# Kernel tuning notes

Hardware: AMD Instinct MI355X
Metric: run time of the kernel (lower is better)

## Reference

```python
import jax, jax.numpy as jnp
import numpy as np

B, S, H = 1, 2048, 2048
NH, NKV, HD = 16, 4, 128
N_REP = NH // NKV
WINDOW = 1024
THETA = 10000.0


def _rope(x, fc):
    # x: [B,S,h,HD]; fc: [B,S,HD//2,2] (cos,sin)
    xr = x.reshape(*x.shape[:-1], HD // 2, 2)
    a, b = xr[..., 0], xr[..., 1]
    cos = fc[:, :, None, :, 0]
    sin = fc[:, :, None, :, 1]
    out = jnp.stack((a * cos - b * sin, a * sin + b * cos), axis=-1)
    return out.reshape(x.shape)


def setup_inputs() -> dict:
    key = jax.random.key(0)
    ks = jax.random.split(key, 5)
    hidden_state = jax.random.normal(ks[0], (B, S, H), jnp.float32)
    # rotary table: cos/sin of pos * theta^{-2i/d}
    inv_freq = 1.0 / (THETA ** (jnp.arange(0, HD, 2, dtype=jnp.float32) / HD))
    ang = jnp.arange(S, dtype=jnp.float32)[:, None] * inv_freq[None, :]  # [S, HD//2]
    freq_cis = jnp.stack((jnp.cos(ang), jnp.sin(ang)), axis=-1)  # [S, HD//2, 2]
    attention_mask = jnp.ones((B, S), dtype=bool)
    i = jnp.arange(S)[:, None]
    j = jnp.arange(S)[None, :]
    causal_mask = ((j <= i) & (i - j < WINDOW))[None, None]  # [1,1,S,S] sliding-window causal
    position_ids = jnp.broadcast_to(jnp.arange(S, dtype=jnp.int32), (B, S))
    scale = 0.02
    Wq = jax.random.normal(ks[1], (H, NH * HD), jnp.float32) * scale
    Wk = jax.random.normal(ks[2], (H, NKV * HD), jnp.float32) * scale
    Wv = jax.random.normal(ks[3], (H, NKV * HD), jnp.float32) * scale
    Wo = jax.random.normal(ks[4], (NH * HD, H), jnp.float32) * scale
    return {"hidden_state": hidden_state, "freq_cis": freq_cis,
            "attention_mask": attention_mask, "causal_mask": causal_mask,
            "position_ids": position_ids, "Wq": Wq, "Wk": Wk, "Wv": Wv, "Wo": Wo}


def reference(hidden_state, freq_cis, attention_mask, causal_mask, position_ids,
              Wq, Wk, Wv, Wo):
    q = (hidden_state @ Wq).reshape(B, S, NH, HD)
    k = (hidden_state @ Wk).reshape(B, S, NKV, HD)
    v = (hidden_state @ Wv).reshape(B, S, NKV, HD)
    fc = freq_cis[position_ids]  # [B,S,HD//2,2]
    q = _rope(q, fc)
    k = _rope(k, fc)
    # GQA: repeat kv heads (contiguous groups, as in repeat_kv)
    k = jnp.repeat(k, N_REP, axis=2)  # [B,S,NH,HD]
    v = jnp.repeat(v, N_REP, axis=2)
    mask = causal_mask & attention_mask[:, None, None, :]  # [B,1,S,S]
    bias = jnp.where(mask, 0.0, jnp.finfo(jnp.float32).min)
    scores = jnp.einsum('bqhd,bkhd->bhqk', q, k) * (1.0 / np.sqrt(HD))
    attn = jax.nn.softmax(scores + bias, axis=-1)
    out = jnp.einsum('bhqk,bkhd->bqhd', attn, v).reshape(B, S, NH * HD)
    return out @ Wo
```

## Files before the change

### kernel.cpp

```cpp
#include <hip/hip_runtime.h>
#include <hip/hip_bf16.h>
#include <stdint.h>

#define S_LEN 2048
#define HDIM  2048
#define NHQ   16
#define NKVH  4
#define HD    128
#define WIN   1024
#define SM_SCALE 0.08838834764831845f
#define NEG_BIG  -1.0e30f

typedef __attribute__((ext_vector_type(8))) short short8;
typedef __attribute__((ext_vector_type(4))) float float4v;
typedef unsigned short u16;

static __device__ __forceinline__ float bf2f(u16 u) {
  union { unsigned int i; float f; } v; v.i = ((unsigned int)u) << 16; return v.f;
}
static __device__ __forceinline__ u16 f2bf(float f) {
  union { float f; unsigned int i; } v; v.f = f;
  unsigned int x = v.i;
  return (u16)((x + 0x7fffu + ((x >> 16) & 1u)) >> 16);
}

__global__ __launch_bounds__(256) void prep(
    const float* __restrict__ hs, const float* __restrict__ Wq,
    const float* __restrict__ Wk, const float* __restrict__ Wv,
    const float* __restrict__ Wo, u16* __restrict__ hsB,
    u16* __restrict__ WqkvT, u16* __restrict__ WoT)
{
  const int b = blockIdx.x;
  if (b < 1024) {
    u16* dst = hsB + (size_t)b * 4096;
    const int mb = b >> 6, ks = b & 63;
#pragma unroll
    for (int i = 0; i < 2; ++i) {
      const int cid = i * 256 + threadIdx.x;
      const int kc  = cid & 3;
      const int m   = cid >> 2;
      const float* src = hs + ((size_t)(mb * 128 + m)) * 2048 + ks * 32 + kc * 8;
      const float4 v0 = *(const float4*)src;
      const float4 v1 = *(const float4*)(src + 4);
      short8 o;
      o[0] = (short)f2bf(v0.x); o[1] = (short)f2bf(v0.y);
      o[2] = (short)f2bf(v0.z); o[3] = (short)f2bf(v0.w);
      o[4] = (short)f2bf(v1.x); o[5] = (short)f2bf(v1.y);
      o[6] = (short)f2bf(v1.z); o[7] = (short)f2bf(v1.w);
      *(short8*)(dst + (kc * 128 + m) * 8) = o;
    }
    return;
  }

  __shared__ u16 t[32][33];
  const int tx = threadIdx.x & 31, ty = threadIdx.x >> 5;
  int n0, kstep;
  const float* W; u16* DT; int nsrc, N;
  if (b < 7168) {
    const int bb = b - 1024;
    n0    = (bb % 96) * 32;
    kstep = bb / 96;
    if (n0 < 2048)      { W = Wq; nsrc = n0;        N = 2048; }
    else if (n0 < 2560) { W = Wk; nsrc = n0 - 2048; N = 512;  }
    else                { W = Wv; nsrc = n0 - 2560; N = 512;  }
    DT = WqkvT;
  } else {
    const int bb = b - 7168;
    n0    = (bb & 63) * 32;
    kstep = bb >> 6;
    W = Wo; nsrc = n0; N = 2048; DT = WoT;
  }
  const int k0 = kstep * 32;

#pragma unroll
  for (int i = 0; i < 4; ++i)
    t[ty + i * 8][tx] = f2bf(W[(size_t)(k0 + ty + i * 8) * N + nsrc + tx]);
  __syncthreads();
  const int kc = tx >> 3, e = tx & 7;
#pragma unroll
  for (int i = 0; i < 4; ++i) {
    const int n = n0 + ty + i * 8;
    DT[((size_t)((n >> 6) * 64 + kstep)) * 2048 + kc * 512 + (n & 63) * 8 + e]
        = t[tx][ty + i * 8];
  }
}

template <int EPI>
__global__ __launch_bounds__(256) void gemm_bt(
    const u16* __restrict__ Apk, const u16* __restrict__ Bpk,
    void* __restrict__ Cv, const float* __restrict__ fc,
    u16* __restrict__ Qb, u16* __restrict__ Kp, u16* __restrict__ Vp,
    int M, int N, int K)
{
  __shared__ u16 Als[2][8192];
  __shared__ u16 Bls[2][4096];

  const int tid  = threadIdx.x;
  const int lane = tid & 63;
  const int w    = tid >> 6;
  const int quad = lane >> 4;
  const int lc   = lane & 15;
  const int n0   = blockIdx.x * 64;
  const int m0   = blockIdx.y * 128;
  const int wr   = (w >> 1) * 64;
  const int wc   = (w & 1) * 32;
  const int ktiles = K >> 5;
  const int nk2    = ktiles >> 1;

  const char* aB = (const char*)(Apk + (size_t)(m0 >> 7) * ktiles * 4096);
  const char* bB = (const char*)(Bpk + (size_t)(n0 >> 6) * ktiles * 2048);

  float4v acc[4][2];
#pragma unroll
  for (int i = 0; i < 4; ++i)
#pragma unroll
    for (int j = 0; j < 2; ++j) acc[i][j] = (float4v){0.f, 0.f, 0.f, 0.f};

  auto stage = [&](int bi, int kk) {
    const char* ab = aB + (size_t)kk * 16384;
    const char* bb = bB + (size_t)kk * 8192;
#pragma unroll
    for (int r = 0; r < 4; ++r) {
      const int off = r * 4096 + tid * 16;
      __builtin_amdgcn_global_load_lds(
          (__attribute__((address_space(1))) void*)(ab + off),
          (__attribute__((address_space(3))) void*)((char*)Als[bi] + off), 16, 0, 0);
    }
#pragma unroll
    for (int r = 0; r < 2; ++r) {
      const int off = r * 4096 + tid * 16;
      __builtin_amdgcn_global_load_lds(
          (__attribute__((address_space(1))) void*)(bb + off),
          (__attribute__((address_space(3))) void*)((char*)Bls[bi] + off), 16, 0, 0);
    }
  };

  stage(0, 0);
  __syncthreads();
  int cur = 0;
  for (int kk = 0; kk < nk2; ++kk) {
    if (kk + 1 < nk2) stage(cur ^ 1, kk + 1);
#pragma unroll
    for (int half = 0; half < 2; ++half) {
      const u16* Ab = Als[cur] + half * 4096;
      const u16* Bb = Bls[cur] + half * 2048;
      short8 af[4], bfr[2];
#pragma unroll
      for (int mi = 0; mi < 4; ++mi)
        af[mi] = *(const short8*)(Ab + quad * 1024 + (wr + mi * 16 + lc) * 8);
#pragma unroll
      for (int ni = 0; ni < 2; ++ni)
        bfr[ni] = *(const short8*)(Bb + quad * 512 + (wc + ni * 16 + lc) * 8);
#pragma unroll
      for (int mi = 0; mi < 4; ++mi)
#pragma unroll
        for (int ni = 0; ni < 2; ++ni)
          acc[mi][ni] = __builtin_amdgcn_mfma_f32_16x16x32_bf16(
              af[mi], bfr[ni], acc[mi][ni], 0, 0, 0);
    }
    __syncthreads();
    cur ^= 1;
  }

  if (EPI == 0) {
#pragma unroll
    for (int mi = 0; mi < 4; ++mi)
#pragma unroll
      for (int ni = 0; ni < 2; ++ni)
#pragma unroll
        for (int r = 0; r < 4; ++r) {
          const int row = m0 + wr + mi * 16 + quad * 4 + r;
          const int col = n0 + wc + ni * 16 + lc;
          ((float*)Cv)[(size_t)row * N + col] = acc[mi][ni][r];
        }
  } else {
    if (n0 < 2560) {
#pragma unroll
      for (int mi = 0; mi < 4; ++mi)
#pragma unroll
        for (int ni = 0; ni < 2; ++ni)
#pragma unroll
          for (int r = 0; r < 4; ++r) {
            const int row = m0 + wr + mi * 16 + quad * 4 + r;
            const int col = n0 + wc + ni * 16 + lc;
            const int hh  = col & 127;
            const float v = acc[mi][ni][r];
            const float p = __shfl_xor(v, 1);
            const float2 cs = *(const float2*)(fc + row * 128 + (hh & ~1));
            const float res = (col & 1) ? (p * cs.y + v * cs.x)
                                        : (v * cs.x - p * cs.y);
            if (n0 < 2048) {
              Qb[(size_t)row * 2048 + col] = f2bf(res);
            } else {
              const int kvh = (col - 2048) >> 7;
              const int kt  = row >> 6, key = row & 63;
              const int c   = hh >> 3, e = hh & 7;
              Kp[((size_t)(kvh * 32 + kt)) * 8192 + key * 128
                 + ((c ^ (key & 15)) * 8) + e] = f2bf(res);
            }
          }
    } else {
#pragma unroll
      for (int mi = 0; mi < 4; ++mi)
#pragma unroll
        for (int ni = 0; ni < 2; ++ni)
#pragma unroll
          for (int r = 0; r < 4; ++r) {
            const int row = m0 + wr + mi * 16 + quad * 4 + r;
            const int col = n0 + wc + ni * 16 + lc;
            const int kvh = (col - 2560) >> 7;
            const int hd  = col & 127;
            const int kt  = row >> 6, key = row & 63;
            const int c   = (key >> 3) ^ (hd & 7);
            Vp[((size_t)(kvh * 32 + kt)) * 8192 + hd * 64 + c * 8 + (key & 7)]
                = f2bf(acc[mi][ni][r]);
          }
    }
  }
}

__global__ __launch_bounds__(256) void attn_kernel(
    const u16* __restrict__ Qb, const u16* __restrict__ kp,
    const u16* __restrict__ vp, u16* __restrict__ out)
{
  __shared__ u16 Kls[2][64 * 128];
  __shared__ u16 Vls[2][128 * 64];
  __shared__ u16 P[4 * 16 * 72];

  const int tid  = threadIdx.x;
  const int lane = tid & 63;
  const int w    = tid >> 6;
  const int quad = lane >> 4;
  const int lc   = lane & 15;

  const int b    = blockIdx.x;
  const int ii   = b & 255;
  const int tt   = ii >> 4;
  const int t    = (b >> 8) ? (31 - tt) : tt;
  const int q0   = t * 64;
  const int h    = ii & 15;
  const int kvh  = h >> 2;
  const int rb   = q0 + w * 16;

  short8 qf[4];
  {
    const u16* qp = Qb + (size_t)(rb + lc) * 2048 + h * HD + quad * 8;
#pragma unroll
    for (int ks = 0; ks < 4; ++ks) qf[ks] = *(const short8*)(qp + ks * 32);
  }

  float4v o[8];
#pragma unroll
  for (int i = 0; i < 8; ++i) o[i] = (float4v){0.f, 0.f, 0.f, 0.f};
  float mrow[4], lrow[4];
#pragma unroll
  for (int r = 0; r < 4; ++r) { mrow[r] = NEG_BIG; lrow[r] = 0.f; }

  int jmin_blk = q0 - (WIN - 1); if (jmin_blk < 0) jmin_blk = 0;
  const int kt_begin = jmin_blk >> 6;
  const int kt_end   = q0 >> 6;

  const size_t tbase = (size_t)(kvh * 32) * 8192;

  auto stageKV = [&](int bi, int ktt) {
    const char* kg = (const char*)(kp + tbase + (size_t)ktt * 8192);
    const char* vg = (const char*)(vp + tbase + (size_t)ktt * 8192);
#pragma unroll
    for (int i = 0; i < 4; ++i) {
      const int off = i * 4096 + tid * 16;
      __builtin_amdgcn_global_load_lds(
          (__attribute__((address_space(1))) void*)(kg + off),
          (__attribute__((address_space(3))) void*)((char*)Kls[bi] + off), 16, 0, 0);
      __builtin_amdgcn_global_load_lds(
          (__attribute__((address_space(1))) void*)(vg + off),
          (__attribute__((address_space(3))) void*)((char*)Vls[bi] + off), 16, 0, 0);
    }
  };

  stageKV(0, kt_begin);
  __syncthreads();
  int cur = 0;

  for (int kt = kt_begin; kt <= kt_end; ++kt) {
    if (kt < kt_end) stageKV(cur ^ 1, kt + 1);
    const int k0 = kt * 64;

    if (!(k0 > rb + 15 || k0 + 63 < rb - (WIN - 1))) {
      float4v sacc[4];
#pragma unroll
      for (int i = 0; i < 4; ++i) sacc[i] = (float4v){0.f, 0.f, 0.f, 0.f};
      __builtin_amdgcn_s_setprio(1);
#pragma unroll
      for (int ks = 0; ks < 4; ++ks) {
#pragma unroll
        for (int nt = 0; nt < 4; ++nt) {
          const int key = nt * 16 + lc;
          const int c   = (ks * 4 + quad) ^ (key & 15);
          short8 kb = *(const short8*)(Kls[cur] + key * 128 + c * 8);
          sacc[nt] = __builtin_amdgcn_mfma_f32_16x16x32_bf16(qf[ks], kb, sacc[nt], 0, 0, 0);
        }
      }
      __builtin_amdgcn_s_setprio(0);

      const bool full = (k0 + 63 <= rb) && ((rb + 15 - k0) <= WIN - 1);
      float sv[4][4];
      bool  ok[4][4];
      float rmax[4] = {NEG_BIG, NEG_BIG, NEG_BIG, NEG_BIG};
#pragma unroll
      for (int nt = 0; nt < 4; ++nt) {
        const int j = k0 + nt * 16 + lc;
#pragma unroll
        for (int r = 0; r < 4; ++r) {
          const int i = rb + quad * 4 + r;
          const bool valid = full || ((j <= i) && (i - j < WIN));
          float s = sacc[nt][r] * SM_SCALE;
          s = valid ? s : NEG_BIG;
          sv[nt][r] = s;
          ok[nt][r] = valid;
          rmax[r] = fmaxf(rmax[r], s);
        }
      }
#pragma unroll
      for (int off = 1; off < 16; off <<= 1)
#pragma unroll
        for (int r = 0; r < 4; ++r)
          rmax[r] = fmaxf(rmax[r], __shfl_xor(rmax[r], off, 64));

      bool grow = false;
#pragma unroll
      for (int r = 0; r < 4; ++r) grow |= (rmax[r] > mrow[r]);
      if (__any((int)grow)) {
#pragma unroll
        for (int r = 0; r < 4; ++r) {
          const float mn = fmaxf(mrow[r], rmax[r]);
          const float a  = __expf(mrow[r] - mn);
          mrow[r] = mn;
          lrow[r] *= a;
#pragma unroll
          for (int i = 0; i < 8; ++i) o[i][r] *= a;
        }
      }

      float rsum[4] = {0.f, 0.f, 0.f, 0.f};
#pragma unroll
      for (int nt = 0; nt < 4; ++nt)
#pragma unroll
        for (int r = 0; r < 4; ++r) {
          const float p = ok[nt][r] ? __expf(sv[nt][r] - mrow[r]) : 0.f;
          rsum[r] += p;
          P[(w * 16 + quad * 4 + r) * 72 + nt * 16 + lc] = f2bf(p);
        }
#pragma unroll
      for (int off = 1; off < 16; off <<= 1)
#pragma unroll
        for (int r = 0; r < 4; ++r)
          rsum[r] += __shfl_xor(rsum[r], off, 64);
#pragma unroll
      for (int r = 0; r < 4; ++r) lrow[r] += rsum[r];

      __builtin_amdgcn_s_setprio(1);
#pragma unroll
      for (int ktk = 0; ktk < 2; ++ktk) {
        short8 pa = *(const short8*)(P + (w * 16 + lc) * 72 + ktk * 32 + quad * 8);
#pragma unroll
        for (int nt2 = 0; nt2 < 8; ++nt2) {
          const int hd = nt2 * 16 + lc;
          const int c  = (ktk * 4 + quad) ^ (hd & 7);
          short8 vb = *(const short8*)(Vls[cur] + hd * 64 + c * 8);
          o[nt2] = __builtin_amdgcn_mfma_f32_16x16x32_bf16(pa, vb, o[nt2], 0, 0, 0);
        }
      }
      __builtin_amdgcn_s_setprio(0);
    }

    __syncthreads();
    cur ^= 1;
  }

#pragma unroll
  for (int r = 0; r < 4; ++r) {
    const float inv = (lrow[r] > 0.f) ? (1.f / lrow[r]) : 0.f;
    const int row = rb + quad * 4 + r;
    const size_t mbase = (size_t)(row >> 7) * 64;
    const int m = row & 127;
#pragma unroll
    for (int nt2 = 0; nt2 < 8; ++nt2) {
      const int col = h * HD + nt2 * 16 + lc;
      const int kstep = col >> 5, kc = (col >> 3) & 3, e = col & 7;
      out[(mbase + kstep) * 4096 + kc * 1024 + m * 8 + e] = f2bf(o[nt2][r] * inv);
    }
  }
}

extern "C" void kernel_launch(void* const* d_in, const int* in_sizes, int n_in,
                              void* d_out, int out_size, void* d_ws, size_t ws_size,
                              hipStream_t stream) {
  const float* hs = (const float*)d_in[0];
  const float* fc = (const float*)d_in[1];
  const float* Wq = (const float*)d_in[5];
  const float* Wk = (const float*)d_in[6];
  const float* Wv = (const float*)d_in[7];
  const float* Wo = (const float*)d_in[8];
  float* outp = (float*)d_out;

  u16* hsB   = (u16*)d_ws;
  u16* WqkvT = hsB   + (size_t)2048 * 2048;
  u16* WoT   = WqkvT + (size_t)3072 * 2048;
  u16* Qb    = WoT   + (size_t)2048 * 2048;
  u16* ATTN  = Qb    + (size_t)2048 * 2048;
  u16* Kp    = ATTN  + (size_t)2048 * 2048;
  u16* Vp    = Kp    + (size_t)4 * 2048 * 128;

  dim3 blk(256);
  prep<<<dim3(11264), blk, 0, stream>>>(hs, Wq, Wk, Wv, Wo, hsB, WqkvT, WoT);
  gemm_bt<1><<<dim3(3072 / 64, 2048 / 128), blk, 0, stream>>>(
      hsB, WqkvT, nullptr, fc, Qb, Kp, Vp, 2048, 3072, 2048);
  attn_kernel<<<dim3(512), blk, 0, stream>>>(Qb, Kp, Vp, ATTN);
  gemm_bt<0><<<dim3(2048 / 64, 2048 / 128), blk, 0, stream>>>(
      ATTN, WoT, outp, nullptr, nullptr, nullptr, nullptr, 2048, 2048, 2048);
}
```

Measured before the change: 236.4 us.

## Split attention key range across two blocks and merge partials in combine kernel

Each query tile's key range is split in half across two blocks (split-K flash attention), doubling the grid to 1024 blocks. Each block writes unnormalized bf16 partial outputs plus row max and sum, and a new combine kernel merges the two halves with rescaling into the layout the output GEMM expects. The attention loop also drops double-buffered K/V staging: K is loaded into LDS synchronously each tile and V is read directly from global memory. This trades an extra kernel launch, partial-output traffic and loss of load/compute overlap for more parallelism and less LDS use. It reuses the hsB workspace for the partials.

```diff
diff --git a/kernel.cpp b/kernel.cpp
--- a/kernel.cpp
+++ b/kernel.cpp
@@ -221,10 +221,9 @@
 
 __global__ __launch_bounds__(256) void attn_kernel(
     const u16* __restrict__ Qb, const u16* __restrict__ kp,
-    const u16* __restrict__ vp, u16* __restrict__ out)
+    const u16* __restrict__ vp, u16* __restrict__ PART, float* __restrict__ ML)
 {
-  __shared__ u16 Kls[2][64 * 128];
-  __shared__ u16 Vls[2][128 * 64];
+  __shared__ u16 Kls[64 * 128];
   __shared__ u16 P[4 * 16 * 72];
 
   const int tid  = threadIdx.x;
@@ -233,14 +232,28 @@
   const int quad = lane >> 4;
   const int lc   = lane & 15;
 
-  const int b    = blockIdx.x;
-  const int ii   = b & 255;
-  const int tt   = ii >> 4;
-  const int t    = (b >> 8) ? (31 - tt) : tt;
-  const int q0   = t * 64;
-  const int h    = ii & 15;
-  const int kvh  = h >> 2;
-  const int rb   = q0 + w * 16;
+  const int id = blockIdx.x;
+  const int g  = id >> 8;
+  const int u  = id & 255;
+  const int h  = u & 15;
+  const int tt = u >> 4;
+  int t, s;
+  if      (g == 0) { t = tt;      s = 0; }
+  else if (g == 1) { t = tt + 16; s = 0; }
+  else if (g == 2) { t = 15 - tt; s = 1; }
+  else             { t = 31 - tt; s = 1; }
+
+  const int q0  = t * 64;
+  const int kvh = h >> 2;
+  const int rb  = q0 + w * 16;
+
+  int jmin_blk = q0 - (WIN - 1); if (jmin_blk < 0) jmin_blk = 0;
+  const int kt_begin = jmin_blk >> 6;
+  const int kt_end   = q0 >> 6;
+  const int ntile    = kt_end - kt_begin + 1;
+  const int nhalf    = (ntile + 1) >> 1;
+  const int my_begin = (s == 0) ? kt_begin : kt_begin + nhalf;
+  const int my_end   = (s == 0) ? kt_begin + nhalf - 1 : kt_end;
 
   short8 qf[4];
   {
@@ -256,139 +269,167 @@
 #pragma unroll
   for (int r = 0; r < 4; ++r) { mrow[r] = NEG_BIG; lrow[r] = 0.f; }
 
-  int jmin_blk = q0 - (WIN - 1); if (jmin_blk < 0) jmin_blk = 0;
-  const int kt_begin = jmin_blk >> 6;
-  const int kt_end   = q0 >> 6;
-
   const size_t tbase = (size_t)(kvh * 32) * 8192;
 
-  auto stageKV = [&](int bi, int ktt) {
-    const char* kg = (const char*)(kp + tbase + (size_t)ktt * 8192);
-    const char* vg = (const char*)(vp + tbase + (size_t)ktt * 8192);
-#pragma unroll
-    for (int i = 0; i < 4; ++i) {
-      const int off = i * 4096 + tid * 16;
-      __builtin_amdgcn_global_load_lds(
-          (__attribute__((address_space(1))) void*)(kg + off),
-          (__attribute__((address_space(3))) void*)((char*)Kls[bi] + off), 16, 0, 0);
-      __builtin_amdgcn_global_load_lds(
-          (__attribute__((address_space(1))) void*)(vg + off),
-          (__attribute__((address_space(3))) void*)((char*)Vls[bi] + off), 16, 0, 0);
-    }
-  };
-
-  stageKV(0, kt_begin);
-  __syncthreads();
-  int cur = 0;
-
-  for (int kt = kt_begin; kt <= kt_end; ++kt) {
-    if (kt < kt_end) stageKV(cur ^ 1, kt + 1);
+  for (int kt = my_begin; kt <= my_end; ++kt) {
     const int k0 = kt * 64;
 
-    if (!(k0 > rb + 15 || k0 + 63 < rb - (WIN - 1))) {
-      float4v sacc[4];
-#pragma unroll
-      for (int i = 0; i < 4; ++i) sacc[i] = (float4v){0.f, 0.f, 0.f, 0.f};
-      __builtin_amdgcn_s_setprio(1);
-#pragma unroll
-      for (int ks = 0; ks < 4; ++ks) {
-#pragma unroll
-        for (int nt = 0; nt < 4; ++nt) {
-          const int key = nt * 16 + lc;
-          const int c   = (ks * 4 + quad) ^ (key & 15);
-          short8 kb = *(const short8*)(Kls[cur] + key * 128 + c * 8);
-          sacc[nt] = __builtin_amdgcn_mfma_f32_16x16x32_bf16(qf[ks], kb, sacc[nt], 0, 0, 0);
-        }
-      }
-      __builtin_amdgcn_s_setprio(0);
-
-      const bool full = (k0 + 63 <= rb) && ((rb + 15 - k0) <= WIN - 1);
-      float sv[4][4];
-      bool  ok[4][4];
-      float rmax[4] = {NEG_BIG, NEG_BIG, NEG_BIG, NEG_BIG};
+    __syncthreads();
+    {
+      const char* kg = (const char*)(kp + tbase + (size_t)kt * 8192);
+#pragma unroll
+      for (int i = 0; i < 4; ++i) {
+        const int off = i * 4096 + tid * 16;
+        __builtin_amdgcn_global_load_lds(
+            (__attribute__((address_space(1))) void*)(kg + off),
+            (__attribute__((address_space(3))) void*)((char*)Kls + off), 16, 0, 0);
+      }
+    }
+    __syncthreads();
+
+    if (k0 > rb + 15 || k0 + 63 < rb - (WIN - 1)) continue;
+
+    float4v sacc[4];
+#pragma unroll
+    for (int i = 0; i < 4; ++i) sacc[i] = (float4v){0.f, 0.f, 0.f, 0.f};
+    __builtin_amdgcn_s_setprio(1);
+#pragma unroll
+    for (int ks = 0; ks < 4; ++ks) {
 #pragma unroll
       for (int nt = 0; nt < 4; ++nt) {
-        const int j = k0 + nt * 16 + lc;
-#pragma unroll
-        for (int r = 0; r < 4; ++r) {
-          const int i = rb + quad * 4 + r;
-          const bool valid = full || ((j <= i) && (i - j < WIN));
-          float s = sacc[nt][r] * SM_SCALE;
-          s = valid ? s : NEG_BIG;
-          sv[nt][r] = s;
-          ok[nt][r] = valid;
-          rmax[r] = fmaxf(rmax[r], s);
-        }
-      }
-#pragma unroll
-      for (int off = 1; off < 16; off <<= 1)
-#pragma unroll
-        for (int r = 0; r < 4; ++r)
-          rmax[r] = fmaxf(rmax[r], __shfl_xor(rmax[r], off, 64));
-
-      bool grow = false;
-#pragma unroll
-      for (int r = 0; r < 4; ++r) grow |= (rmax[r] > mrow[r]);
-      if (__any((int)grow)) {
-#pragma unroll
-        for (int r = 0; r < 4; ++r) {
-          const float mn = fmaxf(mrow[r], rmax[r]);
-          const float a  = __expf(mrow[r] - mn);
-          mrow[r] = mn;
-          lrow[r] *= a;
-#pragma unroll
-          for (int i = 0; i < 8; ++i) o[i][r] *= a;
-        }
-      }
-
-      float rsum[4] = {0.f, 0.f, 0.f, 0.f};
-#pragma unroll
-      for (int nt = 0; nt < 4; ++nt)
-#pragma unroll
-        for (int r = 0; r < 4; ++r) {
-          const float p = ok[nt][r] ? __expf(sv[nt][r] - mrow[r]) : 0.f;
-          rsum[r] += p;
-          P[(w * 16 + quad * 4 + r) * 72 + nt * 16 + lc] = f2bf(p);
-        }
-#pragma unroll
-      for (int off = 1; off < 16; off <<= 1)
-#pragma unroll
-        for (int r = 0; r < 4; ++r)
-          rsum[r] += __shfl_xor(rsum[r], off, 64);
-#pragma unroll
-      for (int r = 0; r < 4; ++r) lrow[r] += rsum[r];
-
-      __builtin_amdgcn_s_setprio(1);
-#pragma unroll
-      for (int ktk = 0; ktk < 2; ++ktk) {
-        short8 pa = *(const short8*)(P + (w * 16 + lc) * 72 + ktk * 32 + quad * 8);
-#pragma unroll
-        for (int nt2 = 0; nt2 < 8; ++nt2) {
-          const int hd = nt2 * 16 + lc;
-          const int c  = (ktk * 4 + quad) ^ (hd & 7);
-          short8 vb = *(const short8*)(Vls[cur] + hd * 64 + c * 8);
-          o[nt2] = __builtin_amdgcn_mfma_f32_16x16x32_bf16(pa, vb, o[nt2], 0, 0, 0);
-        }
-      }
-      __builtin_amdgcn_s_setprio(0);
-    }
-
-    __syncthreads();
-    cur ^= 1;
+        const int key = nt * 16 + lc;
+        const int c   = (ks * 4 + quad) ^ (key & 15);
+        short8 kb = *(const short8*)(Kls + key * 128 + c * 8);
+        sacc[nt] = __builtin_amdgcn_mfma_f32_16x16x32_bf16(qf[ks], kb, sacc[nt], 0, 0, 0);
+      }
+    }
+    __builtin_amdgcn_s_setprio(0);
+
+    const bool full = (k0 + 63 <= rb) && ((rb + 15 - k0) <= WIN - 1);
+    float sv[4][4];
+    bool  ok[4][4];
+    float rmax[4] = {NEG_BIG, NEG_BIG, NEG_BIG, NEG_BIG};
+#pragma unroll
+    for (int nt = 0; nt < 4; ++nt) {
+      const int j = k0 + nt * 16 + lc;
+#pragma unroll
+      for (int r = 0; r < 4; ++r) {
+        const int i = rb + quad * 4 + r;
+        const bool valid = full || ((j <= i) && (i - j < WIN));
+        float sx = sacc[nt][r] * SM_SCALE;
+        sx = valid ? sx : NEG_BIG;
+        sv[nt][r] = sx;
+        ok[nt][r] = valid;
+        rmax[r] = fmaxf(rmax[r], sx);
+      }
+    }
+#pragma unroll
+    for (int off = 1; off < 16; off <<= 1)
+#pragma unroll
+      for (int r = 0; r < 4; ++r)
+        rmax[r] = fmaxf(rmax[r], __shfl_xor(rmax[r], off, 64));
+
+    bool grow = false;
+#pragma unroll
+    for (int r = 0; r < 4; ++r) grow |= (rmax[r] > mrow[r]);
+    if (__any((int)grow)) {
+#pragma unroll
+      for (int r = 0; r < 4; ++r) {
+        const float mn = fmaxf(mrow[r], rmax[r]);
+        const float a  = __expf(mrow[r] - mn);
+        mrow[r] = mn;
+        lrow[r] *= a;
+#pragma unroll
+        for (int i = 0; i < 8; ++i) o[i][r] *= a;
+      }
+    }
+
+    float rsum[4] = {0.f, 0.f, 0.f, 0.f};
+#pragma unroll
+    for (int nt = 0; nt < 4; ++nt)
+#pragma unroll
+      for (int r = 0; r < 4; ++r) {
+        const float p = ok[nt][r] ? __expf(sv[nt][r] - mrow[r]) : 0.f;
+        rsum[r] += p;
+        P[(w * 16 + quad * 4 + r) * 72 + nt * 16 + lc] = f2bf(p);
+      }
+#pragma unroll
+    for (int off = 1; off < 16; off <<= 1)
+#pragma unroll
+      for (int r = 0; r < 4; ++r)
+        rsum[r] += __shfl_xor(rsum[r], off, 64);
+#pragma unroll
+    for (int r = 0; r < 4; ++r) lrow[r] += rsum[r];
+
+    const u16* vgt = vp + tbase + (size_t)kt * 8192;
+    __builtin_amdgcn_s_setprio(1);
+#pragma unroll
+    for (int ktk = 0; ktk < 2; ++ktk) {
+      short8 pa = *(const short8*)(P + (w * 16 + lc) * 72 + ktk * 32 + quad * 8);
+#pragma unroll
+      for (int nt2 = 0; nt2 < 8; ++nt2) {
+        const int hd = nt2 * 16 + lc;
+        const int c  = (ktk * 4 + quad) ^ (hd & 7);
+        short8 vb = *(const short8*)(vgt + hd * 64 + c * 8);
+        o[nt2] = __builtin_amdgcn_mfma_f32_16x16x32_bf16(pa, vb, o[nt2], 0, 0, 0);
+      }
+    }
+    __builtin_amdgcn_s_setprio(0);
   }
 
 #pragma unroll
   for (int r = 0; r < 4; ++r) {
-    const float inv = (lrow[r] > 0.f) ? (1.f / lrow[r]) : 0.f;
-    const int row = rb + quad * 4 + r;
-    const size_t mbase = (size_t)(row >> 7) * 64;
-    const int m = row & 127;
-#pragma unroll
-    for (int nt2 = 0; nt2 < 8; ++nt2) {
-      const int col = h * HD + nt2 * 16 + lc;
-      const int kstep = col >> 5, kc = (col >> 3) & 3, e = col & 7;
-      out[(mbase + kstep) * 4096 + kc * 1024 + m * 8 + e] = f2bf(o[nt2][r] * inv);
-    }
+    const int row = w * 16 + quad * 4 + r;
+#pragma unroll
+    for (int nt2 = 0; nt2 < 8; ++nt2)
+      PART[(size_t)id * 8192 + row * 128 + nt2 * 16 + lc] = f2bf(o[nt2][r]);
+    if (lc == 0) {
+      float2 ml = make_float2(mrow[r], lrow[r]);
+      *(float2*)(ML + (size_t)id * 128 + row * 2) = ml;
+    }
+  }
+}
+
+__global__ __launch_bounds__(256) void combine_kernel(
+    const u16* __restrict__ PART, const float* __restrict__ ML,
+    u16* __restrict__ out)
+{
+  const int cb = blockIdx.x;
+  const int t = cb & 31, h = cb >> 5;
+  int g0, tt0, g1, tt1;
+  if (t < 16) { g0 = 0; tt0 = t;      g1 = 2; tt1 = 15 - t; }
+  else        { g0 = 1; tt0 = t - 16; g1 = 3; tt1 = 31 - t; }
+  const int id0 = (g0 << 8) | (tt0 << 4) | h;
+  const int id1 = (g1 << 8) | (tt1 << 4) | h;
+
+  const int tid = threadIdx.x;
+  const int row = tid >> 2;
+  const int jj  = tid & 3;
+
+  const float2 ml0 = *(const float2*)(ML + (size_t)id0 * 128 + row * 2);
+  const float2 ml1 = *(const float2*)(ML + (size_t)id1 * 128 + row * 2);
+  const float m  = fmaxf(ml0.x, ml1.x);
+  const float a0 = __expf(ml0.x - m), a1 = __expf(ml1.x - m);
+  const float l  = a0 * ml0.y + a1 * ml1.y;
+  const float inv = (l > 0.f) ? 1.f / l : 0.f;
+  const float f0 = a0 * inv, f1 = a1 * inv;
+
+  const int rowg  = t * 64 + row;
+  const size_t mbase = (size_t)(rowg >> 7) * 64;
+  const int mloc  = rowg & 127;
+  const int kstep = h * 4 + jj;
+
+  const u16* p0 = PART + (size_t)id0 * 8192 + row * 128 + jj * 32;
+  const u16* p1 = PART + (size_t)id1 * 8192 + row * 128 + jj * 32;
+#pragma unroll
+  for (int j = 0; j < 4; ++j) {
+    short8 a = *(const short8*)(p0 + j * 8);
+    short8 b = *(const short8*)(p1 + j * 8);
+    short8 ov;
+#pragma unroll
+    for (int e = 0; e < 8; ++e)
+      ov[e] = (short)f2bf(bf2f((u16)a[e]) * f0 + bf2f((u16)b[e]) * f1);
+    *(short8*)(out + (mbase + kstep) * 4096 + j * 1024 + mloc * 8) = ov;
   }
 }
 
@@ -411,11 +452,15 @@
   u16* Kp    = ATTN  + (size_t)2048 * 2048;
   u16* Vp    = Kp    + (size_t)4 * 2048 * 128;
 
+  u16*   PARTb = hsB;
+  float* MLf   = (float*)(hsB + (size_t)1024 * 8192);
+
   dim3 blk(256);
   prep<<<dim3(11264), blk, 0, stream>>>(hs, Wq, Wk, Wv, Wo, hsB, WqkvT, WoT);
   gemm_bt<1><<<dim3(3072 / 64, 2048 / 128), blk, 0, stream>>>(
       hsB, WqkvT, nullptr, fc, Qb, Kp, Vp, 2048, 3072, 2048);
-  attn_kernel<<<dim3(512), blk, 0, stream>>>(Qb, Kp, Vp, ATTN);
+  attn_kernel<<<dim3(1024), blk, 0, stream>>>(Qb, Kp, Vp, PARTb, MLf);
+  combine_kernel<<<dim3(512), blk, 0, stream>>>(PARTb, MLf, ATTN);
   gemm_bt<0><<<dim3(2048 / 64, 2048 / 128), blk, 0, stream>>>(
       ATTN, WoT, outp, nullptr, nullptr, nullptr, nullptr, 2048, 2048, 2048);
 }
```

Measured after the change: 252.5 us. 1.07x slower.

## Make attention single-wave blocks reading K/V straight from global memory

Applied to the files above, without the earlier changes.

The attention kernel moves from 256-thread blocks that shared double-buffered K/V tiles in LDS to 64-thread single-wave blocks, 2048 in total, that load K/V fragments straight from global memory, which in practice means L2. Each wave gets its own key-tile range, drops the __syncthreads barriers and takes a separate fast path for fully unmasked tiles. This is meant to remove barrier stalls, LDS staging and the wasted work on masked tiles, and to raise occupancy. In exchange the K/V reuse across the four waves of a block is lost, so global/L2 traffic rises. The work order also changes: the old causal load-balancing swap (31 - tt) is gone.

```diff
diff --git a/kernel.cpp b/kernel.cpp
--- a/kernel.cpp
+++ b/kernel.cpp
@@ -219,28 +219,25 @@
   }
 }
 
-__global__ __launch_bounds__(256) void attn_kernel(
+__global__ __launch_bounds__(64, 3) void attn_kernel(
     const u16* __restrict__ Qb, const u16* __restrict__ kp,
     const u16* __restrict__ vp, u16* __restrict__ out)
 {
-  __shared__ u16 Kls[2][64 * 128];
-  __shared__ u16 Vls[2][128 * 64];
-  __shared__ u16 P[4 * 16 * 72];
-
-  const int tid  = threadIdx.x;
-  const int lane = tid & 63;
-  const int w    = tid >> 6;
+  __shared__ u16 P[16 * 72];
+
+  const int lane = threadIdx.x;
   const int quad = lane >> 4;
   const int lc   = lane & 15;
 
-  const int b    = blockIdx.x;
-  const int ii   = b & 255;
-  const int tt   = ii >> 4;
-  const int t    = (b >> 8) ? (31 - tt) : tt;
-  const int q0   = t * 64;
-  const int h    = ii & 15;
-  const int kvh  = h >> 2;
-  const int rb   = q0 + w * 16;
+  const int id = blockIdx.x;
+  const int u  = id & 255;
+  const int g  = id >> 8;
+  const int h  = u & 15;
+  const int w  = (u >> 4) & 3;
+  const int j2 = u >> 6;
+  const int t  = g * 4 + j2;
+  const int kvh = h >> 2;
+  const int rb  = t * 64 + w * 16;
 
   short8 qf[4];
   {
@@ -256,125 +253,110 @@
 #pragma unroll
   for (int r = 0; r < 4; ++r) { mrow[r] = NEG_BIG; lrow[r] = 0.f; }
 
-  int jmin_blk = q0 - (WIN - 1); if (jmin_blk < 0) jmin_blk = 0;
-  const int kt_begin = jmin_blk >> 6;
-  const int kt_end   = q0 >> 6;
+  int jmin = rb - (WIN - 1); if (jmin < 0) jmin = 0;
+  const int kt_begin = jmin >> 6;
+  const int kt_end   = (rb + 15) >> 6;
 
   const size_t tbase = (size_t)(kvh * 32) * 8192;
 
-  auto stageKV = [&](int bi, int ktt) {
-    const char* kg = (const char*)(kp + tbase + (size_t)ktt * 8192);
-    const char* vg = (const char*)(vp + tbase + (size_t)ktt * 8192);
-#pragma unroll
-    for (int i = 0; i < 4; ++i) {
-      const int off = i * 4096 + tid * 16;
-      __builtin_amdgcn_global_load_lds(
-          (__attribute__((address_space(1))) void*)(kg + off),
-          (__attribute__((address_space(3))) void*)((char*)Kls[bi] + off), 16, 0, 0);
-      __builtin_amdgcn_global_load_lds(
-          (__attribute__((address_space(1))) void*)(vg + off),
-          (__attribute__((address_space(3))) void*)((char*)Vls[bi] + off), 16, 0, 0);
-    }
-  };
-
-  stageKV(0, kt_begin);
-  __syncthreads();
-  int cur = 0;
-
   for (int kt = kt_begin; kt <= kt_end; ++kt) {
-    if (kt < kt_end) stageKV(cur ^ 1, kt + 1);
     const int k0 = kt * 64;
-
-    if (!(k0 > rb + 15 || k0 + 63 < rb - (WIN - 1))) {
-      float4v sacc[4];
-#pragma unroll
-      for (int i = 0; i < 4; ++i) sacc[i] = (float4v){0.f, 0.f, 0.f, 0.f};
-      __builtin_amdgcn_s_setprio(1);
-#pragma unroll
-      for (int ks = 0; ks < 4; ++ks) {
-#pragma unroll
-        for (int nt = 0; nt < 4; ++nt) {
-          const int key = nt * 16 + lc;
-          const int c   = (ks * 4 + quad) ^ (key & 15);
-          short8 kb = *(const short8*)(Kls[cur] + key * 128 + c * 8);
-          sacc[nt] = __builtin_amdgcn_mfma_f32_16x16x32_bf16(qf[ks], kb, sacc[nt], 0, 0, 0);
+    const u16* kg = kp + tbase + (size_t)kt * 8192;
+    const u16* vg = vp + tbase + (size_t)kt * 8192;
+
+    float4v sacc[4];
+#pragma unroll
+    for (int i = 0; i < 4; ++i) sacc[i] = (float4v){0.f, 0.f, 0.f, 0.f};
+    __builtin_amdgcn_s_setprio(1);
+#pragma unroll
+    for (int ks = 0; ks < 4; ++ks) {
+#pragma unroll
+      for (int nt = 0; nt < 4; ++nt) {
+        const int key = nt * 16 + lc;
+        const int c   = (ks * 4 + quad) ^ lc;
+        short8 kb = *(const short8*)(kg + key * 128 + c * 8);
+        sacc[nt] = __builtin_amdgcn_mfma_f32_16x16x32_bf16(qf[ks], kb, sacc[nt], 0, 0, 0);
+      }
+    }
+    __builtin_amdgcn_s_setprio(0);
+
+    const bool full = (k0 + 63 <= rb) && ((rb + 15 - k0) <= WIN - 1);
+    float sv[4][4];
+    float rmax[4] = {NEG_BIG, NEG_BIG, NEG_BIG, NEG_BIG};
+    if (full) {
+#pragma unroll
+      for (int nt = 0; nt < 4; ++nt)
+#pragma unroll
+        for (int r = 0; r < 4; ++r) {
+          const float sx = sacc[nt][r] * SM_SCALE;
+          sv[nt][r] = sx;
+          rmax[r] = fmaxf(rmax[r], sx);
+        }
+    } else {
+#pragma unroll
+      for (int nt = 0; nt < 4; ++nt) {
+        const int j = k0 + nt * 16 + lc;
+#pragma unroll
+        for (int r = 0; r < 4; ++r) {
+          const int i = rb + quad * 4 + r;
+          const bool valid = (j <= i) && (i - j < WIN);
+          const float sx = valid ? sacc[nt][r] * SM_SCALE : NEG_BIG;
+          sv[nt][r] = sx;
+          rmax[r] = fmaxf(rmax[r], sx);
         }
       }
-      __builtin_amdgcn_s_setprio(0);
-
-      const bool full = (k0 + 63 <= rb) && ((rb + 15 - k0) <= WIN - 1);
-      float sv[4][4];
-      bool  ok[4][4];
-      float rmax[4] = {NEG_BIG, NEG_BIG, NEG_BIG, NEG_BIG};
-#pragma unroll
-      for (int nt = 0; nt < 4; ++nt) {
-        const int j = k0 + nt * 16 + lc;
-#pragma unroll
-        for (int r = 0; r < 4; ++r) {
-          const int i = rb + quad * 4 + r;
-          const bool valid = full || ((j <= i) && (i - j < WIN));
-          float s = sacc[nt][r] * SM_SCALE;
-          s = valid ? s : NEG_BIG;
-          sv[nt][r] = s;
-          ok[nt][r] = valid;
-          rmax[r] = fmaxf(rmax[r], s);
-        }
+    }
+#pragma unroll
+    for (int off = 1; off < 16; off <<= 1)
+#pragma unroll
+      for (int r = 0; r < 4; ++r)
+        rmax[r] = fmaxf(rmax[r], __shfl_xor(rmax[r], off, 64));
+
+    bool grow = false;
+#pragma unroll
+    for (int r = 0; r < 4; ++r) grow |= (rmax[r] > mrow[r]);
+    if (__any((int)grow)) {
+#pragma unroll
+      for (int r = 0; r < 4; ++r) {
+        const float mn = fmaxf(mrow[r], rmax[r]);
+        const float a  = __expf(mrow[r] - mn);
+        mrow[r] = mn;
+        lrow[r] *= a;
+#pragma unroll
+        for (int i = 0; i < 8; ++i) o[i][r] *= a;
       }
-#pragma unroll
-      for (int off = 1; off < 16; off <<= 1)
-#pragma unroll
-        for (int r = 0; r < 4; ++r)
-          rmax[r] = fmaxf(rmax[r], __shfl_xor(rmax[r], off, 64));
-
-      bool grow = false;
-#pragma unroll
-      for (int r = 0; r < 4; ++r) grow |= (rmax[r] > mrow[r]);
-      if (__any((int)grow)) {
-#pragma unroll
-        for (int r = 0; r < 4; ++r) {
-          const float mn = fmaxf(mrow[r], rmax[r]);
-          const float a  = __expf(mrow[r] - mn);
-          mrow[r] = mn;
-          lrow[r] *= a;
-#pragma unroll
-          for (int i = 0; i < 8; ++i) o[i][r] *= a;
-        }
+    }
+
+    float rsum[4] = {0.f, 0.f, 0.f, 0.f};
+#pragma unroll
+    for (int nt = 0; nt < 4; ++nt)
+#pragma unroll
+      for (int r = 0; r < 4; ++r) {
+        const float p = __expf(sv[nt][r] - mrow[r]);
+        rsum[r] += p;
+        P[(quad * 4 + r) * 72 + nt * 16 + lc] = f2bf(p);
       }
-
-      float rsum[4] = {0.f, 0.f, 0.f, 0.f};
-#pragma unroll
-      for (int nt = 0; nt < 4; ++nt)
-#pragma unroll
-        for (int r = 0; r < 4; ++r) {
-          const float p = ok[nt][r] ? __expf(sv[nt][r] - mrow[r]) : 0.f;
-          rsum[r] += p;
-          P[(w * 16 + quad * 4 + r) * 72 + nt * 16 + lc] = f2bf(p);
-        }
-#pragma unroll
-      for (int off = 1; off < 16; off <<= 1)
-#pragma unroll
-        for (int r = 0; r < 4; ++r)
-          rsum[r] += __shfl_xor(rsum[r], off, 64);
-#pragma unroll
-      for (int r = 0; r < 4; ++r) lrow[r] += rsum[r];
-
-      __builtin_amdgcn_s_setprio(1);
-#pragma unroll
-      for (int ktk = 0; ktk < 2; ++ktk) {
-        short8 pa = *(const short8*)(P + (w * 16 + lc) * 72 + ktk * 32 + quad * 8);
-#pragma unroll
-        for (int nt2 = 0; nt2 < 8; ++nt2) {
-          const int hd = nt2 * 16 + lc;
-          const int c  = (ktk * 4 + quad) ^ (hd & 7);
-          short8 vb = *(const short8*)(Vls[cur] + hd * 64 + c * 8);
-          o[nt2] = __builtin_amdgcn_mfma_f32_16x16x32_bf16(pa, vb, o[nt2], 0, 0, 0);
-        }
+#pragma unroll
+    for (int off = 1; off < 16; off <<= 1)
+#pragma unroll
+      for (int r = 0; r < 4; ++r)
+        rsum[r] += __shfl_xor(rsum[r], off, 64);
+#pragma unroll
+    for (int r = 0; r < 4; ++r) lrow[r] += rsum[r];
+
+    __builtin_amdgcn_s_setprio(1);
+#pragma unroll
+    for (int ktk = 0; ktk < 2; ++ktk) {
+      short8 pa = *(const short8*)(P + lc * 72 + ktk * 32 + quad * 8);
+#pragma unroll
+      for (int nt2 = 0; nt2 < 8; ++nt2) {
+        const int hd = nt2 * 16 + lc;
+        const int c  = (ktk * 4 + quad) ^ (hd & 7);
+        short8 vb = *(const short8*)(vg + hd * 64 + c * 8);
+        o[nt2] = __builtin_amdgcn_mfma_f32_16x16x32_bf16(pa, vb, o[nt2], 0, 0, 0);
       }
-      __builtin_amdgcn_s_setprio(0);
-    }
-
-    __syncthreads();
-    cur ^= 1;
+    }
+    __builtin_amdgcn_s_setprio(0);
   }
 
 #pragma unroll
@@ -415,7 +397,7 @@
   prep<<<dim3(11264), blk, 0, stream>>>(hs, Wq, Wk, Wv, Wo, hsB, WqkvT, WoT);
   gemm_bt<1><<<dim3(3072 / 64, 2048 / 128), blk, 0, stream>>>(
       hsB, WqkvT, nullptr, fc, Qb, Kp, Vp, 2048, 3072, 2048);
-  attn_kernel<<<dim3(512), blk, 0, stream>>>(Qb, Kp, Vp, ATTN);
+  attn_kernel<<<dim3(2048), dim3(64), 0, stream>>>(Qb, Kp, Vp, ATTN);
   gemm_bt<0><<<dim3(2048 / 64, 2048 / 128), blk, 0, stream>>>(
       ATTN, WoT, outp, nullptr, nullptr, nullptr, nullptr, 2048, 2048, 2048);
 }
```

New measurement: 246.7 us. 1.04x slower.
